# Performance work log

Hardware: AMD Instinct MI355X
Metric: run time of the kernel (lower is better)

The kernel has to match this reference:

```python
import jax, jax.numpy as jnp
import numpy as np

S, B, D = 2048, 2, 1024
H, KV = 16, 4
HD = D // H          # 64
N_REP = H // KV      # 4
EPS = 1e-5
THETA = 10000.0
SCALE = D ** -0.5    # qk_norm_scale = 0.03125 (use_qk_norm path)


def rms_norm(x, w, eps=EPS):
    return x / jnp.sqrt(jnp.mean(x * x, axis=-1, keepdims=True) + eps) * w


def rotate_half(x):
    x1, x2 = jnp.split(x, 2, axis=-1)
    return jnp.concatenate((-x2, x1), axis=-1)


def rope_tables(seq_len, dim, theta=THETA):
    inv_freq = 1.0 / (theta ** (jnp.arange(0, dim, 2, dtype=jnp.float32) / dim))
    t = jnp.arange(seq_len, dtype=jnp.float32)
    freqs = jnp.outer(t, inv_freq)                 # [S, dim/2]
    emb = jnp.concatenate((freqs, freqs), axis=-1)  # [S, dim]
    return jnp.cos(emb), jnp.sin(emb)


def setup_inputs() -> dict:
    key = jax.random.key(0)
    ks = jax.random.split(key, 16)
    s = lambda fan_in: fan_in ** -0.5
    return {
        "x": jax.random.normal(ks[0], (S, B, D), jnp.float32),
        "norm1_w": jnp.ones((D,), jnp.float32),
        "wq": jax.random.normal(ks[1], (D, H * HD), jnp.float32) * s(D),
        "bq": jnp.zeros((H * HD,), jnp.float32),
        "wk": jax.random.normal(ks[2], (D, KV * HD), jnp.float32) * s(D),
        "bk": jnp.zeros((KV * HD,), jnp.float32),
        "wv": jax.random.normal(ks[3], (D, KV * HD), jnp.float32) * s(D),
        "bv": jnp.zeros((KV * HD,), jnp.float32),
        "qn_w": jnp.ones((HD,), jnp.float32),
        "kn_w": jnp.ones((HD,), jnp.float32),
        "wo": jax.random.normal(ks[4], (D, D), jnp.float32) * s(D),
        "bo": jnp.zeros((D,), jnp.float32),
        "norm2_w": jnp.ones((D,), jnp.float32),
        "w1": jax.random.normal(ks[5], (D, 4 * D), jnp.float32) * s(D),
        "b1": jnp.zeros((4 * D,), jnp.float32),
        "w2": jax.random.normal(ks[6], (4 * D, D), jnp.float32) * s(4 * D),
        "b2": jnp.zeros((D,), jnp.float32),
    }


def reference(x, norm1_w, wq, bq, wk, bk, wv, bv, qn_w, kn_w, wo, bo,
              norm2_w, w1, b1, w2, b2):
    # x: [S, B, D] (seq-first, TE convention)
    residual = x
    h = rms_norm(x, norm1_w)
    q = (h @ wq + bq).reshape(S, B, H, HD).transpose(1, 2, 0, 3)    # [B,H,S,HD]
    k = (h @ wk + bk).reshape(S, B, KV, HD).transpose(1, 2, 0, 3)   # [B,KV,S,HD]
    v = (h @ wv + bv).reshape(S, B, KV, HD).transpose(1, 2, 0, 3)
    # GQA: repeat_interleave over head dim
    k = jnp.repeat(k, N_REP, axis=1)  # [B,H,S,HD]
    v = jnp.repeat(v, N_REP, axis=1)
    # per-head QK RMSNorm
    q = rms_norm(q, qn_w)
    k = rms_norm(k, kn_w)
    # RoPE
    cos, sin = rope_tables(S, HD)          # [S,HD] each
    cos = cos[None, None]                  # [1,1,S,HD]
    sin = sin[None, None]
    q = q * cos + rotate_half(q) * sin
    k = k * cos + rotate_half(k) * sin
    # attention with explicit causal mask
    scores = jnp.einsum('bhsd,bhtd->bhst', q, k) * SCALE
    causal = jnp.triu(jnp.ones((S, S), bool), k=1)
    scores = jnp.where(causal, -jnp.inf, scores)
    attn = jax.nn.softmax(scores, axis=-1)
    out = jnp.einsum('bhst,bhtd->bhsd', attn, v)       # [B,H,S,HD]
    out = out.transpose(0, 2, 1, 3).reshape(B, S, D)   # [B,S,D]
    out = out.transpose(1, 0, 2)                       # [S,B,D]
    out = out @ wo + bo
    x = residual + out
    # MLP block (RMSNorm + GELU MLP)
    residual = x
    h2 = rms_norm(x, norm2_w)
    h2 = jax.nn.gelu(h2 @ w1 + b1, approximate=False) @ w2 + b2
    return residual + h2
```

## Files before the change

kernel.cpp:

```cpp
#include <hip/hip_runtime.h>
#include <hip/hip_bf16.h>
#include <math.h>

#define S_LEN 2048
#define BATCH 2
#define DMODEL 1024
#define NH 16
#define NKV 4
#define HDIM 64
#define EPS 1e-5f
#define MROWS (S_LEN*BATCH)
#define QSCALE (0.03125f * 1.44269504088896f)

#define AS1 __attribute__((address_space(1)))
#define AS3 __attribute__((address_space(3)))

typedef __attribute__((ext_vector_type(8))) short bf8_t;
typedef __attribute__((ext_vector_type(4))) float f4_t;
typedef _Float16 __attribute__((ext_vector_type(8))) h8_t;
typedef _Float16 __attribute__((ext_vector_type(4))) h4_t;

#define MFMA16(a,b,c) __builtin_amdgcn_mfma_f32_16x16x16f16(a,b,c,0,0,0)

__device__ __forceinline__ float exp2_fast(float x){ return __builtin_exp2f(x); }

__device__ __forceinline__ unsigned short f2bf(float f){
  __hip_bfloat16 b = __float2bfloat16(f);
  return __builtin_bit_cast(unsigned short, b);
}
__device__ __forceinline__ float bf2f(unsigned short u){
  return __builtin_bit_cast(float, (unsigned)u << 16);
}
__device__ __forceinline__ float gelu_f(float x){
  return 0.5f * x * (1.0f + erff(x * 0.7071067811865475f));
}

__global__ __launch_bounds__(256) void prep_k(const float* __restrict__ wq, const float* __restrict__ wk,
                                              const float* __restrict__ wv, const float* __restrict__ wo,
                                              const float* __restrict__ w1, const float* __restrict__ w2,
                                              __hip_bfloat16* __restrict__ wqkv_t, __hip_bfloat16* __restrict__ wo_t,
                                              __hip_bfloat16* __restrict__ w1_t,   __hip_bfloat16* __restrict__ w2_t,
                                              const float* __restrict__ x, const float* __restrict__ n1w,
                                              __hip_bfloat16* __restrict__ h){
  if (blockIdx.x < 10752){
    __shared__ float t[32][33];
    int b = blockIdx.x;
    const float* src; __hip_bfloat16* dst; int N, stride, nx;
    if (b < 1024)      { src=wq; dst=wqkv_t;               N=1024; stride=1024; nx=32;  }
    else if (b < 1280) { b-=1024; src=wk; dst=wqkv_t+1024*1024; N=256; stride=1024; nx=8; }
    else if (b < 1536) { b-=1280; src=wv; dst=wqkv_t+1280*1024; N=256; stride=1024; nx=8; }
    else if (b < 2560) { b-=1536; src=wo; dst=wo_t;        N=1024; stride=1024; nx=32;  }
    else if (b < 6656) { b-=2560; src=w1; dst=w1_t;        N=4096; stride=1024; nx=128; }
    else               { b-=6656; src=w2; dst=w2_t;        N=1024; stride=4096; nx=32;  }
    int n0 = (b % nx)*32, k0 = (b / nx)*32;
    int tx = threadIdx.x & 31, ty = threadIdx.x >> 5;
    #pragma unroll
    for (int i = 0; i < 4; ++i)
      t[ty*4+i][tx] = src[(size_t)(k0+ty*4+i)*N + n0 + tx];
    __syncthreads();
    #pragma unroll
    for (int i = 0; i < 4; ++i)
      dst[(size_t)(n0+ty*4+i)*stride + k0 + tx] = __float2bfloat16(t[tx][ty*4+i]);
  } else {
    __shared__ float sm[5];
    size_t row = blockIdx.x - 10752;
    const float4* xr = (const float4*)(x + row * DMODEL);
    float4 v = xr[threadIdx.x];
    float ss = v.x*v.x + v.y*v.y + v.z*v.z + v.w*v.w;
    #pragma unroll
    for (int off = 32; off; off >>= 1) ss += __shfl_down(ss, off);
    if ((threadIdx.x & 63) == 0) sm[threadIdx.x >> 6] = ss;
    __syncthreads();
    if (threadIdx.x == 0) sm[4] = rsqrtf((sm[0]+sm[1]+sm[2]+sm[3]) * (1.0f/DMODEL) + EPS);
    __syncthreads();
    float r = sm[4];
    float4 wv4 = ((const float4*)n1w)[threadIdx.x];
    ushort4 ob;
    ob.x = f2bf(v.x*r*wv4.x); ob.y = f2bf(v.y*r*wv4.y);
    ob.z = f2bf(v.z*r*wv4.z); ob.w = f2bf(v.w*r*wv4.w);
    ((ushort4*)(h + row * DMODEL))[threadIdx.x] = ob;
  }
}

template<int EPI>
__global__ __launch_bounds__(256) void mgemm_k(const __hip_bfloat16* __restrict__ A,
                                               const __hip_bfloat16* __restrict__ Wt,
                                               const float* __restrict__ bias,
                                               __hip_bfloat16* __restrict__ Cb,
                                               int N, int Kstride, int kLen){
  __shared__ __align__(16) __hip_bfloat16 As[2][8192];
  __shared__ __align__(16) __hip_bfloat16 Bs[2][8192];
  const int tid = threadIdx.x;
  const int w = tid >> 6, l = tid & 63;
  const int lr = l & 15, lc = l >> 4;
  const int bm = blockIdx.y * 128, bn = blockIdx.x * 128;
  const int wm = (w >> 1) * 64, wn = (w & 1) * 64;
  const int kOff = blockIdx.z * kLen;

  const __hip_bfloat16* Ag = A  + (size_t)(bm + 2*w*16 + lr)*Kstride + kOff + lc*8;
  const __hip_bfloat16* Bg = Wt + (size_t)(bn + 2*w*16 + lr)*Kstride + kOff + lc*8;

  f4_t acc[4][4] = {};

  const int nt = kLen >> 6;

  auto stage = [&](int buf, int k0){
    #pragma unroll
    for (int rg = 0; rg < 2; ++rg)
      #pragma unroll
      for (int j = 0; j < 2; ++j){
        __builtin_amdgcn_global_load_lds((const AS1 void*)(Ag + rg*16*(size_t)Kstride + k0 + j*32),
                                         (AS3 void*)(&As[buf][(2*w+rg)*1024 + j*512 + l*8]), 16, 0, 0);
        __builtin_amdgcn_global_load_lds((const AS1 void*)(Bg + rg*16*(size_t)Kstride + k0 + j*32),
                                         (AS3 void*)(&Bs[buf][(2*w+rg)*1024 + j*512 + l*8]), 16, 0, 0);
      }
  };

  stage(0, 0);
  asm volatile("s_waitcnt vmcnt(0)" ::: "memory");
  __builtin_amdgcn_s_barrier();

  int cur = 0;
  for (int t = 0; t < nt; ++t){
    if (t + 1 < nt) stage(cur ^ 1, (t + 1) << 6);

    #pragma unroll
    for (int s = 0; s < 2; ++s){
      bf8_t af[4], bfr[4];
      #pragma unroll
      for (int mi = 0; mi < 4; ++mi)
        af[mi] = *(const bf8_t*)(&As[cur][((wm>>4)+mi)*1024 + s*512 + l*8]);
      #pragma unroll
      for (int ni = 0; ni < 4; ++ni)
        bfr[ni] = *(const bf8_t*)(&Bs[cur][((wn>>4)+ni)*1024 + s*512 + l*8]);
      #pragma unroll
      for (int mi = 0; mi < 4; ++mi)
        #pragma unroll
        for (int ni = 0; ni < 4; ++ni)
          acc[mi][ni] = __builtin_amdgcn_mfma_f32_16x16x32_bf16(af[mi], bfr[ni], acc[mi][ni], 0, 0, 0);
    }

    asm volatile("s_waitcnt vmcnt(0)" ::: "memory");
    __builtin_amdgcn_s_barrier();
    cur ^= 1;
  }

  __hip_bfloat16* Cp = (EPI == 3) ? (Cb + (size_t)blockIdx.z * ((size_t)MROWS * N)) : Cb;

  #pragma unroll
  for (int ni = 0; ni < 4; ++ni){
    int col = bn + wn + ni*16 + lr;
    float bb = (EPI == 3) ? 0.0f : bias[col];
    #pragma unroll
    for (int mi = 0; mi < 4; ++mi){
      #pragma unroll
      for (int r = 0; r < 4; ++r){
        int row = bm + wm + mi*16 + lc*4 + r;
        size_t off = (size_t)row * N + col;
        float v = acc[mi][ni][r] + bb;
        if (EPI == 1) Cp[off] = __float2bfloat16(gelu_f(v));
        else          Cp[off] = __float2bfloat16(v);
      }
    }
  }
}

template<int NS>
__global__ __launch_bounds__(256) void reduce_k(const unsigned short* __restrict__ P,
                                                const float* __restrict__ bias,
                                                const float* __restrict__ res,
                                                float* __restrict__ out, int N){
  size_t i = ((size_t)blockIdx.x*256 + threadIdx.x) * 4;
  int col = (int)(i % (size_t)N);
  size_t stride = (size_t)MROWS * N;
  float a0=0,a1=0,a2=0,a3=0;
  #pragma unroll
  for (int p = 0; p < NS; ++p){
    ushort4 u = *(const ushort4*)(P + p*stride + i);
    a0 += bf2f(u.x); a1 += bf2f(u.y); a2 += bf2f(u.z); a3 += bf2f(u.w);
  }
  float4 bb = *(const float4*)(bias + col);
  float4 r4 = *(const float4*)(res + i);
  float4 o = make_float4(a0+bb.x+r4.x, a1+bb.y+r4.y, a2+bb.z+r4.z, a3+bb.w+r4.w);
  *(float4*)(out + i) = o;
}

template<int NS>
__global__ __launch_bounds__(256) void redn_k(const unsigned short* __restrict__ P,
                                              const float* __restrict__ bias,
                                              const float* __restrict__ res,
                                              const float* __restrict__ nw,
                                              float* __restrict__ x1,
                                              __hip_bfloat16* __restrict__ h){
  __shared__ float sm[5];
  size_t row = blockIdx.x;
  size_t i = row * DMODEL + threadIdx.x*4;
  size_t stride = (size_t)MROWS * DMODEL;
  float4 bb = *(const float4*)(bias + threadIdx.x*4);
  float4 r4 = *(const float4*)(res + i);
  float4 v = make_float4(bb.x+r4.x, bb.y+r4.y, bb.z+r4.z, bb.w+r4.w);
  #pragma unroll
  for (int p = 0; p < NS; ++p){
    ushort4 u = *(const ushort4*)(P + p*stride + i);
    v.x += bf2f(u.x); v.y += bf2f(u.y); v.z += bf2f(u.z); v.w += bf2f(u.w);
  }
  *(float4*)(x1 + i) = v;
  float ss = v.x*v.x + v.y*v.y + v.z*v.z + v.w*v.w;
  #pragma unroll
  for (int off = 32; off; off >>= 1) ss += __shfl_down(ss, off);
  if ((threadIdx.x & 63) == 0) sm[threadIdx.x >> 6] = ss;
  __syncthreads();
  if (threadIdx.x == 0) sm[4] = rsqrtf((sm[0]+sm[1]+sm[2]+sm[3]) * (1.0f/DMODEL) + EPS);
  __syncthreads();
  float r = sm[4];
  float4 wv = ((const float4*)nw)[threadIdx.x];
  ushort4 ob;
  ob.x = f2bf(v.x*r*wv.x); ob.y = f2bf(v.y*r*wv.y);
  ob.z = f2bf(v.z*r*wv.z); ob.w = f2bf(v.w*r*wv.w);
  ((ushort4*)(h + row * DMODEL))[threadIdx.x] = ob;
}

__global__ __launch_bounds__(64) void rope2_k(const unsigned short* __restrict__ P,
                                              const float* __restrict__ bq, const float* __restrict__ bk,
                                              const float* __restrict__ qw, const float* __restrict__ kw,
                                              _Float16* __restrict__ qo, _Float16* __restrict__ ko){
  const int s = blockIdx.x;
  const int y = blockIdx.y;
  const int b = y / 20, r0 = y % 20;
  const bool isQ = (r0 < 16);
  const int hh = isQ ? r0 : (r0 - 16);
  const int col0 = isQ ? hh*64 : 1024 + hh*64;
  const int lane = threadIdx.x;
  const size_t pstride = (size_t)MROWS * 1536;
  size_t off = ((size_t)s * BATCH + b) * 1536 + col0 + lane;
  float v = bf2f(P[off]) + bf2f(P[off + pstride])
          + (isQ ? bq[hh*64 + lane] : bk[hh*64 + lane]);
  float ss = v * v;
  #pragma unroll
  for (int m = 32; m; m >>= 1) ss += __shfl_xor(ss, m);
  float rr = rsqrtf(ss * (1.0f/64.0f) + EPS);
  v = v * rr * (isQ ? qw[lane] : kw[lane]);
  int i = lane & 31;
  float invf = powf(10000.0f, -((float)(2*i)) * (1.0f/64.0f));
  float ang = (float)s * invf;
  float c, sn;
  sincosf(ang, &sn, &c);
  float partner = __shfl_xor(v, 32);
  float rh = (lane < 32) ? -partner : partner;
  float o = (v * c + rh * sn) * (isQ ? QSCALE : 1.0f);
  _Float16* outp = isQ ? (qo + (((size_t)b * NH  + hh) * S_LEN + s) * 64 + lane)
                       : (ko + (((size_t)b * NKV + hh) * S_LEN + s) * 64 + lane);
  *outp = (_Float16)o;
}

__global__ __launch_bounds__(256) void vcast_k(const unsigned short* __restrict__ P,
                                               const float* __restrict__ bv,
                                               _Float16* __restrict__ Vt){
  __shared__ float t[64][65];
  const int s0 = blockIdx.x * 64;
  const int bkv = blockIdx.y;
  const int b = bkv >> 2, kv = bkv & 3;
  const int tid = threadIdx.x;
  const size_t pstride = (size_t)MROWS * 1536;
  #pragma unroll
  for (int i = 0; i < 16; ++i){
    int idx = tid + 256*i;
    int sl = idx >> 6, d = idx & 63;
    size_t off = ((size_t)(s0+sl)*BATCH + b)*1536 + 1280 + kv*64 + d;
    t[d][sl] = bf2f(P[off]) + bf2f(P[off + pstride]) + bv[kv*64 + d];
  }
  __syncthreads();
  #pragma unroll
  for (int i = 0; i < 16; ++i){
    int idx = tid + 256*i;
    int d = idx >> 6, sl = idx & 63;
    Vt[((size_t)bkv*64 + d)*S_LEN + s0 + sl] = (_Float16)t[d][sl];
  }
}

__global__ __launch_bounds__(256) void attn2_k(const _Float16* __restrict__ Q,
                                               const _Float16* __restrict__ K,
                                               const _Float16* __restrict__ Vt,
                                               __hip_bfloat16* __restrict__ AO){
  __shared__ __align__(16) _Float16 Ks[8*512];
  __shared__ __align__(16) _Float16 Vs[8*512];
  const int bh = blockIdx.x;
  const int qb = (gridDim.y - 1) - blockIdx.y;
  const int b = bh >> 4, h = bh & 15;
  const int kvh = h >> 2;
  const int tid = threadIdx.x;
  const int w = tid >> 6, l = tid & 63;
  const int lr = l & 15, quad = l >> 4;

  const _Float16* qp = Q + ((size_t)bh * S_LEN + qb*64 + w*16 + lr) * 64;
  h8_t qf0 = *(const h8_t*)(qp + quad*8);
  h8_t qf1 = *(const h8_t*)(qp + 32 + quad*8);

  const _Float16* kbase = K  + (size_t)(b*NKV + kvh) * S_LEN * 64;
  const _Float16* vbase = Vt + (size_t)(b*NKV + kvh) * 64 * S_LEN;

  f4_t Od[4] = {};
  float m_i = -3.0e38f, l_i = 0.0f;

  for (int kt = 0; kt <= qb; ++kt){
    __syncthreads();
    #pragma unroll
    for (int ii = 0; ii < 4; ++ii){
      int i = w*4 + ii;
      if (i < 8){
        int cc = i >> 1, dh = i & 1;
        const _Float16* src = kbase + (size_t)(kt*64 + cc*16 + lr)*64 + dh*32 + quad*8;
        __builtin_amdgcn_global_load_lds((const AS1 void*)src, (AS3 void*)(Ks + i*512), 16, 0, 0);
      } else {
        int j = i - 8;
        int dd = j >> 1, cc32 = j & 1;
        const _Float16* src = vbase + (size_t)(dd*16 + lr)*S_LEN + kt*64 + cc32*32 + quad*8;
        __builtin_amdgcn_global_load_lds((const AS1 void*)src, (AS3 void*)(Vs + j*512), 16, 0, 0);
      }
    }
    __syncthreads();

    const bool diag = (kt == qb);
    f4_t sc[4];
    #pragma unroll
    for (int nc2 = 0; nc2 < 4; ++nc2){
      if (diag && nc2 > w){
        sc[nc2][0] = -1.0e30f; sc[nc2][1] = -1.0e30f;
        sc[nc2][2] = -1.0e30f; sc[nc2][3] = -1.0e30f;
        continue;
      }
      f4_t a = {};
      h8_t k0 = *(const h8_t*)(Ks + (nc2*2+0)*512 + l*8);
      h8_t k1 = *(const h8_t*)(Ks + (nc2*2+1)*512 + l*8);
      a = __builtin_amdgcn_mfma_f32_16x16x32_f16(k0, qf0, a, 0, 0, 0);
      a = __builtin_amdgcn_mfma_f32_16x16x32_f16(k1, qf1, a, 0, 0, 0);
      if (diag && nc2 == w){
        #pragma unroll
        for (int r = 0; r < 4; ++r)
          if (quad*4 + r > lr) a[r] = -1.0e30f;
      }
      sc[nc2] = a;
    }

    float mx = sc[0][0];
    #pragma unroll
    for (int nc2 = 0; nc2 < 4; ++nc2)
      #pragma unroll
      for (int r = 0; r < 4; ++r) mx = fmaxf(mx, sc[nc2][r]);
    mx = fmaxf(mx, __shfl_xor(mx, 16));
    mx = fmaxf(mx, __shfl_xor(mx, 32));
    float nm = fmaxf(mx, m_i);
    float alpha = exp2_fast(m_i - nm);
    m_i = nm;
    float rs = 0.0f;
    h4_t pf[4];
    #pragma unroll
    for (int nc2 = 0; nc2 < 4; ++nc2)
      #pragma unroll
      for (int r = 0; r < 4; ++r){
        float e = exp2_fast(sc[nc2][r] - nm);
        rs += e;
        pf[nc2][r] = (_Float16)e;
      }
    rs += __shfl_xor(rs, 16);
    rs += __shfl_xor(rs, 32);
    l_i = l_i * alpha + rs;
    #pragma unroll
    for (int dd = 0; dd < 4; ++dd)
      #pragma unroll
      for (int r = 0; r < 4; ++r) Od[dd][r] *= alpha;

    #pragma unroll
    for (int dd = 0; dd < 4; ++dd)
      #pragma unroll
      for (int nc2 = 0; nc2 < 4; ++nc2){
        if (diag && nc2 > w) continue;
        h4_t vf = *(const h4_t*)(Vs + (dd*2 + (nc2>>1))*512
                                 + (((nc2&1)*2 + (quad>>1))*16 + lr)*8 + (quad&1)*4);
        Od[dd] = MFMA16(vf, pf[nc2], Od[dd]);
      }
  }

  float inv = 1.0f / l_i;
  #pragma unroll
  for (int dd = 0; dd < 4; ++dd){
    ushort4 w4;
    w4.x = f2bf(Od[dd][0]*inv); w4.y = f2bf(Od[dd][1]*inv);
    w4.z = f2bf(Od[dd][2]*inv); w4.w = f2bf(Od[dd][3]*inv);
    size_t sg = (size_t)qb*64 + w*16 + lr;
    *(ushort4*)(AO + (sg*BATCH + b)*DMODEL + h*64 + dd*16 + quad*4) = w4;
  }
}

extern "C" void kernel_launch(void* const* d_in, const int* in_sizes, int n_in,
                              void* d_out, int out_size, void* d_ws, size_t ws_size,
                              hipStream_t stream){
  const float* x   = (const float*)d_in[0];
  const float* n1w = (const float*)d_in[1];
  const float* wq  = (const float*)d_in[2];
  const float* bq  = (const float*)d_in[3];
  const float* wk  = (const float*)d_in[4];
  const float* bk  = (const float*)d_in[5];
  const float* wv  = (const float*)d_in[6];
  const float* bv  = (const float*)d_in[7];
  const float* qnw = (const float*)d_in[8];
  const float* knw = (const float*)d_in[9];
  const float* wo  = (const float*)d_in[10];
  const float* bo  = (const float*)d_in[11];
  const float* n2w = (const float*)d_in[12];
  const float* w1  = (const float*)d_in[13];
  const float* b1  = (const float*)d_in[14];
  const float* w2  = (const float*)d_in[15];
  const float* b2  = (const float*)d_in[16];
  float* out = (float*)d_out;

  char* p = (char*)d_ws;
  auto carve = [&](size_t bytes)->char*{ char* r = p; p += (bytes + 255) & ~(size_t)255; return r; };
  __hip_bfloat16* h_bf   = (__hip_bfloat16*)carve((size_t)MROWS*DMODEL*2);
  __hip_bfloat16* ao_bf  = (__hip_bfloat16*)carve((size_t)MROWS*DMODEL*2);
  __hip_bfloat16* mid_bf = (__hip_bfloat16*)carve((size_t)MROWS*4096*2);
  __hip_bfloat16* wqkv_t = (__hip_bfloat16*)carve((size_t)1536*1024*2);
  __hip_bfloat16* wo_t   = (__hip_bfloat16*)carve((size_t)1024*1024*2);
  __hip_bfloat16* w1_t   = (__hip_bfloat16*)carve((size_t)4096*1024*2);
  __hip_bfloat16* w2_t   = (__hip_bfloat16*)carve((size_t)1024*4096*2);
  char* scratch = carve((size_t)2*MROWS*1536*2);
  __hip_bfloat16* qkv_p = (__hip_bfloat16*)scratch;
  __hip_bfloat16* ps    = (__hip_bfloat16*)scratch;
  _Float16* q_f  = (_Float16*)carve((size_t)BATCH*NH *S_LEN*64*2);
  _Float16* k_f  = (_Float16*)carve((size_t)BATCH*NKV*S_LEN*64*2);
  _Float16* vt_f = (_Float16*)carve((size_t)BATCH*NKV*64*S_LEN*2);
  float* x1   = (float*)carve((size_t)MROWS*DMODEL*4);

  prep_k<<<10752 + MROWS, 256, 0, stream>>>(wq, wk, wv, wo, w1, w2,
                                            wqkv_t, wo_t, w1_t, w2_t, x, n1w, h_bf);

  mgemm_k<3><<<dim3(12, 32, 2), 256, 0, stream>>>(h_bf, wqkv_t, nullptr, qkv_p, 1536, 1024, 512);

  rope2_k<<<dim3(S_LEN, BATCH*20), 64, 0, stream>>>((const unsigned short*)qkv_p, bq, bk, qnw, knw, q_f, k_f);
  vcast_k<<<dim3(S_LEN/64, BATCH*NKV), 256, 0, stream>>>((const unsigned short*)qkv_p, bv, vt_f);
  attn2_k<<<dim3(BATCH*NH, S_LEN/64), 256, 0, stream>>>(q_f, k_f, vt_f, ao_bf);

  mgemm_k<3><<<dim3(8, 32, 2), 256, 0, stream>>>(ao_bf, wo_t, nullptr, ps, 1024, 1024, 512);
  redn_k<2><<<MROWS, 256, 0, stream>>>((const unsigned short*)ps, bo, x, n2w, x1, h_bf);

  mgemm_k<1><<<dim3(32, 32, 1), 256, 0, stream>>>(h_bf, w1_t, b1, mid_bf, 4096, 1024, 1024);

  mgemm_k<3><<<dim3(8, 32, 2), 256, 0, stream>>>(mid_bf, w2_t, nullptr, ps, 1024, 4096, 2048);
  reduce_k<2><<<4096, 256, 0, stream>>>((const unsigned short*)ps, b2, x1, out, 1024);
}
```

Before: 431.0 us.

## Remap GEMM block indices for XCD locality; single-buffer the W2 GEMM

```diff
diff --git a/kernel.cpp b/kernel.cpp
--- a/kernel.cpp
+++ b/kernel.cpp
@@ -82,27 +82,33 @@
   }
 }
 
-template<int EPI>
+template<int EPI, bool DB>
 __global__ __launch_bounds__(256) void mgemm_k(const __hip_bfloat16* __restrict__ A,
                                                const __hip_bfloat16* __restrict__ Wt,
                                                const float* __restrict__ bias,
                                                __hip_bfloat16* __restrict__ Cb,
                                                int N, int Kstride, int kLen){
-  __shared__ __align__(16) __hip_bfloat16 As[2][8192];
-  __shared__ __align__(16) __hip_bfloat16 Bs[2][8192];
+  __shared__ __align__(16) __hip_bfloat16 As[DB?2:1][8192];
+  __shared__ __align__(16) __hip_bfloat16 Bs[DB?2:1][8192];
   const int tid = threadIdx.x;
   const int w = tid >> 6, l = tid & 63;
   const int lr = l & 15, lc = l >> 4;
-  const int bm = blockIdx.y * 128, bn = blockIdx.x * 128;
+
+  const unsigned gx = gridDim.x, gy = gridDim.y;
+  unsigned hb  = (blockIdx.z * gy + blockIdx.y) * gx + blockIdx.x;
+  unsigned cpx = (gx * gy * gridDim.z) >> 3;
+  unsigned role = (hb & 7u) * cpx + (hb >> 3);
+  unsigned bxi = role % gx; unsigned t2 = role / gx;
+  unsigned byi = t2 % gy;   unsigned bzi = t2 / gy;
+
+  const int bm = byi * 128, bn = bxi * 128;
   const int wm = (w >> 1) * 64, wn = (w & 1) * 64;
-  const int kOff = blockIdx.z * kLen;
+  const int kOff = bzi * kLen;
 
   const __hip_bfloat16* Ag = A  + (size_t)(bm + 2*w*16 + lr)*Kstride + kOff + lc*8;
   const __hip_bfloat16* Bg = Wt + (size_t)(bn + 2*w*16 + lr)*Kstride + kOff + lc*8;
 
   f4_t acc[4][4] = {};
-
-  const int nt = kLen >> 6;
 
   auto stage = [&](int buf, int k0){
     #pragma unroll
@@ -116,36 +122,47 @@
       }
   };
 
-  stage(0, 0);
-  asm volatile("s_waitcnt vmcnt(0)" ::: "memory");
-  __builtin_amdgcn_s_barrier();
-
-  int cur = 0;
-  for (int t = 0; t < nt; ++t){
-    if (t + 1 < nt) stage(cur ^ 1, (t + 1) << 6);
-
+  auto compute = [&](int buf){
     #pragma unroll
     for (int s = 0; s < 2; ++s){
       bf8_t af[4], bfr[4];
       #pragma unroll
       for (int mi = 0; mi < 4; ++mi)
-        af[mi] = *(const bf8_t*)(&As[cur][((wm>>4)+mi)*1024 + s*512 + l*8]);
+        af[mi] = *(const bf8_t*)(&As[buf][((wm>>4)+mi)*1024 + s*512 + l*8]);
       #pragma unroll
       for (int ni = 0; ni < 4; ++ni)
-        bfr[ni] = *(const bf8_t*)(&Bs[cur][((wn>>4)+ni)*1024 + s*512 + l*8]);
+        bfr[ni] = *(const bf8_t*)(&Bs[buf][((wn>>4)+ni)*1024 + s*512 + l*8]);
       #pragma unroll
       for (int mi = 0; mi < 4; ++mi)
         #pragma unroll
         for (int ni = 0; ni < 4; ++ni)
           acc[mi][ni] = __builtin_amdgcn_mfma_f32_16x16x32_bf16(af[mi], bfr[ni], acc[mi][ni], 0, 0, 0);
     }
-
+  };
+
+  if constexpr (DB){
+    const int nt = kLen >> 6;
+    stage(0, 0);
     asm volatile("s_waitcnt vmcnt(0)" ::: "memory");
     __builtin_amdgcn_s_barrier();
-    cur ^= 1;
-  }
-
-  __hip_bfloat16* Cp = (EPI == 3) ? (Cb + (size_t)blockIdx.z * ((size_t)MROWS * N)) : Cb;
+    int cur = 0;
+    for (int t = 0; t < nt; ++t){
+      if (t + 1 < nt) stage(cur ^ 1, (t + 1) << 6);
+      compute(cur);
+      asm volatile("s_waitcnt vmcnt(0)" ::: "memory");
+      __builtin_amdgcn_s_barrier();
+      cur ^= 1;
+    }
+  } else {
+    for (int k0 = 0; k0 < kLen; k0 += 64){
+      __syncthreads();
+      stage(0, k0);
+      __syncthreads();
+      compute(0);
+    }
+  }
+
+  __hip_bfloat16* Cp = (EPI == 3) ? (Cb + (size_t)bzi * ((size_t)MROWS * N)) : Cb;
 
   #pragma unroll
   for (int ni = 0; ni < 4; ++ni){
@@ -434,17 +451,17 @@
   prep_k<<<10752 + MROWS, 256, 0, stream>>>(wq, wk, wv, wo, w1, w2,
                                             wqkv_t, wo_t, w1_t, w2_t, x, n1w, h_bf);
 
-  mgemm_k<3><<<dim3(12, 32, 2), 256, 0, stream>>>(h_bf, wqkv_t, nullptr, qkv_p, 1536, 1024, 512);
+  mgemm_k<3,true><<<dim3(12, 32, 2), 256, 0, stream>>>(h_bf, wqkv_t, nullptr, qkv_p, 1536, 1024, 512);
 
   rope2_k<<<dim3(S_LEN, BATCH*20), 64, 0, stream>>>((const unsigned short*)qkv_p, bq, bk, qnw, knw, q_f, k_f);
   vcast_k<<<dim3(S_LEN/64, BATCH*NKV), 256, 0, stream>>>((const unsigned short*)qkv_p, bv, vt_f);
   attn2_k<<<dim3(BATCH*NH, S_LEN/64), 256, 0, stream>>>(q_f, k_f, vt_f, ao_bf);
 
-  mgemm_k<3><<<dim3(8, 32, 2), 256, 0, stream>>>(ao_bf, wo_t, nullptr, ps, 1024, 1024, 512);
+  mgemm_k<3,true><<<dim3(8, 32, 2), 256, 0, stream>>>(ao_bf, wo_t, nullptr, ps, 1024, 1024, 512);
   redn_k<2><<<MROWS, 256, 0, stream>>>((const unsigned short*)ps, bo, x, n2w, x1, h_bf);
 
-  mgemm_k<1><<<dim3(32, 32, 1), 256, 0, stream>>>(h_bf, w1_t, b1, mid_bf, 4096, 1024, 1024);
-
-  mgemm_k<3><<<dim3(8, 32, 2), 256, 0, stream>>>(mid_bf, w2_t, nullptr, ps, 1024, 4096, 2048);
+  mgemm_k<1,true><<<dim3(32, 32, 1), 256, 0, stream>>>(h_bf, w1_t, b1, mid_bf, 4096, 1024, 1024);
+
+  mgemm_k<3,false><<<dim3(8, 32, 2), 256, 0, stream>>>(mid_bf, w2_t, nullptr, ps, 1024, 4096, 2048);
   reduce_k<2><<<4096, 256, 0, stream>>>((const unsigned short*)ps, b2, x1, out, 1024);
 }
```

After: 425.1 us. No clear change (-1.4%).
